# Optimization experiments

Measured on AMD Instinct MI355X. Metric: run time of the kernel, lower is better.

Reference implementation:

```python
import jax, jax.numpy as jnp
import numpy as np

B, N, H = 16, 1024, 768
NEG_INF = -9e15
SLOPE = 0.2


def setup_inputs() -> dict:
    key = jax.random.key(0)
    k1, k2, k3, k4, k5 = jax.random.split(key, 5)
    x = jax.random.normal(k1, (B, N, H), dtype=jnp.float32)
    # node_length acts as a per-node validity mask (float, used via outer product)
    lengths = jax.random.randint(k2, (B,), N // 2, N)
    node_length = (jnp.arange(N)[None, :] < lengths[:, None]).astype(jnp.float32)
    # sparse-ish binary adjacency with self-loops
    adj = (jax.random.uniform(k3, (B, N, N)) < 0.05).astype(jnp.float32)
    adj = jnp.maximum(adj, jnp.eye(N, dtype=jnp.float32)[None])
    # params: kaiming-normal init
    W = jax.random.normal(k4, (H, H), dtype=jnp.float32) * np.sqrt(2.0 / H)
    a = jax.random.normal(k5, (2 * H, 1), dtype=jnp.float32) * np.sqrt(2.0 / (2 * H))
    return {"input": x, "node_length": node_length, "graph_structure": adj, "W": W, "a": a}


def reference(input, node_length, graph_structure, W, a):
    # node_vec = A @ X  [B,N,H]
    node_vec = jnp.matmul(graph_structure, input)
    h = jnp.matmul(node_vec, W)  # [B,N,F]
    F_ = W.shape[1]
    a1 = a[:F_, 0]   # weights on h_i
    a2 = a[F_:, 0]   # weights on h_j
    # e[b,i,j] = leaky_relu(h_i . a1 + h_j . a2)  (identical to concat+matmul with a)
    s1 = jnp.einsum("bnf,f->bn", h, a1)
    s2 = jnp.einsum("bnf,f->bn", h, a2)
    e = jax.nn.leaky_relu(s1[:, :, None] + s2[:, None, :], negative_slope=SLOPE)
    # bias = outer product of node_length; mask where adj or bias <= 1e-6
    bias = node_length[:, :, None] * node_length[:, None, :]
    valid = (graph_structure > 1e-6) & (bias > 1e-6)
    scores = jnp.where(valid, e, NEG_INF)
    attn = jax.nn.softmax(scores, axis=-1)  # attn_dropout=0 -> identity
    return node_vec, attn
```

## Files before the change

kernel.cpp:

```cpp
#include <hip/hip_runtime.h>
#include <hip/hip_bf16.h>

#define BB 16
#define NN 1024
#define HH 768
#define NEG_INF_ -9.0e15f
#define SLOPE_ 0.2f

typedef __bf16 bh8 __attribute__((ext_vector_type(8)));
typedef __bf16 bh4 __attribute__((ext_vector_type(4)));
typedef float f4 __attribute__((ext_vector_type(4)));
typedef unsigned int u32;
typedef unsigned long long u64;


__device__ __forceinline__ float wave_sum0(float v) {
    #pragma unroll
    for (int off = 32; off > 0; off >>= 1) v += __shfl_down(v, off, 64);
    return v;
}
__device__ __forceinline__ float wave_sum_all(float v) {
    #pragma unroll
    for (int off = 1; off < 64; off <<= 1) v += __shfl_xor(v, off, 64);
    return v;
}
__device__ __forceinline__ float wave_max_all(float v) {
    #pragma unroll
    for (int off = 1; off < 64; off <<= 1) v = fmaxf(v, __shfl_xor(v, off, 64));
    return v;
}


__device__ __forceinline__ void gl_lds16(const void* g, void* l) {
    __builtin_amdgcn_global_load_lds(
        (const __attribute__((address_space(1))) u32*)g,
        (__attribute__((address_space(3))) u32*)l, 16, 0, 0);
}


__global__ __launch_bounds__(256) void wa_kernel(const float* __restrict__ W,
                                                 const float* __restrict__ a,
                                                 float* __restrict__ wa1,
                                                 float* __restrict__ wa2) {
    const int f = blockIdx.x * 4 + (threadIdx.x >> 6);
    const int lane = threadIdx.x & 63;
    const float* Wr = W + (size_t)f * HH;
    float v1 = 0.f, v2 = 0.f;
    #pragma unroll
    for (int i = 0; i < 3; i++) {
        const int h = lane * 4 + i * 256;
        const float4 w  = *(const float4*)(Wr + h);
        const float4 a1 = *(const float4*)(a + h);
        const float4 a2 = *(const float4*)(a + HH + h);
        v1 += w.x * a1.x + w.y * a1.y + w.z * a1.z + w.w * a1.w;
        v2 += w.x * a2.x + w.y * a2.y + w.z * a2.z + w.w * a2.w;
    }
    v1 = wave_sum0(v1);
    v2 = wave_sum0(v2);
    if (lane == 0) { wa1[f] = v1; wa2[f] = v2; }
}


__global__ __launch_bounds__(256) void t_kernel(const float* __restrict__ x,
                                                const float* __restrict__ wa1,
                                                const float* __restrict__ wa2,
                                                float* __restrict__ t1,
                                                float* __restrict__ t2) {
    const int row = blockIdx.x * 4 + (threadIdx.x >> 6);
    const int lane = threadIdx.x & 63;
    const float* xr = x + (size_t)row * HH;
    float v1 = 0.f, v2 = 0.f;
    #pragma unroll
    for (int i = 0; i < 3; i++) {
        const int h = lane * 4 + i * 256;
        const float4 xv = *(const float4*)(xr + h);
        const float4 w1 = *(const float4*)(wa1 + h);
        const float4 w2 = *(const float4*)(wa2 + h);
        v1 += xv.x * w1.x + xv.y * w1.y + xv.z * w1.z + xv.w * w1.w;
        v2 += xv.x * w2.x + xv.y * w2.y + xv.z * w2.z + xv.w * w2.w;
    }
    v1 = wave_sum0(v1);
    v2 = wave_sum0(v2);
    if (lane == 0) { t1[row] = v1; t2[row] = v2; }
}


__global__ __launch_bounds__(256) void xt_kernel(const float* __restrict__ x,
                                                 __bf16* __restrict__ xT) {
    __shared__ __bf16 T[32][36];
    const int b = blockIdx.z, nt = blockIdx.y, ht = blockIdx.x;
    const int t = threadIdx.x;
    {
        const int r = t >> 3;
        const int c = (t & 7) * 4;
        const float4 v = *(const float4*)(x + ((size_t)b * NN + nt * 32 + r) * HH + ht * 32 + c);
        T[r][c + 0] = (__bf16)v.x; T[r][c + 1] = (__bf16)v.y;
        T[r][c + 2] = (__bf16)v.z; T[r][c + 3] = (__bf16)v.w;
    }
    __syncthreads();
    {
        const int h = t >> 3;
        const int nc = (t & 7) * 4;
        bh4 o = { T[nc + 0][h], T[nc + 1][h], T[nc + 2][h], T[nc + 3][h] };
        *(bh4*)(xT + ((size_t)b * HH + ht * 32 + h) * NN + nt * 32 + nc) = o;
    }
}


__global__ __launch_bounds__(256) void s_pack_kernel(const float* __restrict__ adj,
                                                     const float* __restrict__ t1,
                                                     const float* __restrict__ t2,
                                                     float* __restrict__ s1,
                                                     float* __restrict__ s2,
                                                     u64* __restrict__ bits) {
    const int row = blockIdx.x * 4 + (threadIdx.x >> 6);
    const int lane = threadIdx.x & 63;
    const int b = row >> 10;
    const float* ar = adj + (size_t)row * NN;
    const float* t1b = t1 + b * NN;
    const float* t2b = t2 + b * NN;
    float v1 = 0.f, v2 = 0.f;
    u64 myw = 0;
    #pragma unroll
    for (int i = 0; i < 16; i++) {
        const int m = lane + 64 * i;
        const float av = ar[m];
        v1 += av * t1b[m];
        v2 += av * t2b[m];
        const u64 bal = __ballot(av > 1e-6f);
        if (lane == i) myw = bal;
    }
    v1 = wave_sum0(v1);
    v2 = wave_sum0(v2);
    if (lane == 0) { s1[row] = v1; s2[row] = v2; }
    if (lane < 16) bits[(size_t)row * 16 + lane] = myw;
}


__global__ __launch_bounds__(256) void softmax_kernel(const float* __restrict__ adj,
                                                      const float* __restrict__ nl,
                                                      const float* __restrict__ s1,
                                                      const float* __restrict__ s2,
                                                      float* __restrict__ attn) {
    const int row = blockIdx.x * 4 + (threadIdx.x >> 6);
    const int lane = threadIdx.x & 63;
    const int b = row >> 10, n = row & (NN - 1);
    const float* ar = adj + (size_t)row * NN;
    const float* nlb = nl + (size_t)b * NN;
    const float* s2b = s2 + (size_t)b * NN;
    const float s1v = s1[row];
    const bool rowok = nlb[n] > 1e-6f;

    f4 sc[4];
    float mx = NEG_INF_;
    #pragma unroll
    for (int i = 0; i < 4; i++) {
        const int j = lane * 4 + i * 256;
        const float4 av = *(const float4*)(ar + j);
        const float4 sv = *(const float4*)(s2b + j);
        const float4 nv = *(const float4*)(nlb + j);
        const float zs[4] = { s1v + sv.x, s1v + sv.y, s1v + sv.z, s1v + sv.w };
        const float as_[4] = { av.x, av.y, av.z, av.w };
        const float ns[4] = { nv.x, nv.y, nv.z, nv.w };
        #pragma unroll
        for (int e = 0; e < 4; e++) {
            const float z = zs[e];
            const float lr = z > 0.f ? z : SLOPE_ * z;
            const bool valid = rowok && (as_[e] > 1e-6f) && (ns[e] > 1e-6f);
            sc[i][e] = valid ? lr : NEG_INF_;
            mx = fmaxf(mx, sc[i][e]);
        }
    }
    mx = wave_max_all(mx);

    f4 ex[4];
    float sum = 0.f;
    #pragma unroll
    for (int i = 0; i < 4; i++)
        #pragma unroll
        for (int e = 0; e < 4; e++) {
            ex[i][e] = __expf(sc[i][e] - mx);
            sum += ex[i][e];
        }
    sum = wave_sum_all(sum);
    const float inv = 1.0f / sum;

    float* outr = attn + (size_t)row * NN;
    #pragma unroll
    for (int i = 0; i < 4; i++) {
        const int j = lane * 4 + i * 256;
        float4 o;
        o.x = ex[i][0] * inv; o.y = ex[i][1] * inv;
        o.z = ex[i][2] * inv; o.w = ex[i][3] * inv;
        *(float4*)(outr + j) = o;
    }
}


#define BSTRIDE 36

__global__ __launch_bounds__(256) void gemm_bits(const u32* __restrict__ bits,
                                                 const __bf16* __restrict__ xT,
                                                 float* __restrict__ out) {
    __shared__ u32 bitsL[128 * BSTRIDE];
    __shared__ __bf16 Bs[128 * 32];
    const int b = blockIdx.z, bm = blockIdx.y, bn = blockIdx.x;
    const int tid = threadIdx.x, lane = tid & 63, wave = tid >> 6;
    const int wr = (wave >> 1) << 6;
    const int wc = (wave & 1) << 6;
    const int quad = lane >> 4, l16 = lane & 15;

    const u32* bg = bits + ((size_t)b * NN + bm * 128) * 32;
    #pragma unroll
    for (int it = 0; it < 4; it++) {
        const int c = tid + 256 * it;
        const int r = c >> 3, col = (c & 7) * 4;
        const uint4 v = *(const uint4*)(bg + r * 32 + col);
        *(uint4*)&bitsL[r * BSTRIDE + col] = v;
    }

    f4 acc[4][4];
    #pragma unroll
    for (int i = 0; i < 4; i++)
        #pragma unroll
        for (int j = 0; j < 4; j++)
            acc[i][j] = (f4){0.f, 0.f, 0.f, 0.f};

    const __bf16* xb = xT + ((size_t)b * HH + bn * 128) * NN;
    __syncthreads();

    for (int kt = 0; kt < NN; kt += 32) {
        #pragma unroll
        for (int it = 0; it < 2; it++) {
            const int c = tid + 256 * it;
            const int n = c >> 2, off = (c & 3) * 16;
            gl_lds16((const char*)(xb + (size_t)n * NN + kt) + off,
                     (char*)&Bs[n * 32] + off);
        }
        __syncthreads();

        bh8 af[4], bf_[4];
        const int kw = kt >> 5;
        #pragma unroll
        for (int i = 0; i < 4; i++) {
            const u32 w = bitsL[(wr + i * 16 + l16) * BSTRIDE + kw];
            const u32 byte = (w >> (quad * 8)) & 0xffu;
            #pragma unroll
            for (int j = 0; j < 8; j++)
                af[i][j] = ((byte >> j) & 1u) ? (__bf16)1.0f : (__bf16)0.0f;
        }
        #pragma unroll
        for (int j = 0; j < 4; j++)
            bf_[j] = *(const bh8*)&Bs[(wc + j * 16 + l16) * 32 + quad * 8];

        #pragma unroll
        for (int i = 0; i < 4; i++)
            #pragma unroll
            for (int j = 0; j < 4; j++)
                acc[i][j] = __builtin_amdgcn_mfma_f32_16x16x32_bf16(af[i], bf_[j], acc[i][j], 0, 0, 0);
        __syncthreads();
    }

    float* Cb = out + (size_t)b * NN * HH + (size_t)bm * 128 * HH + bn * 128;
    const int rbase = wr + quad * 4;
    const int cbase = wc + l16;
    #pragma unroll
    for (int i = 0; i < 4; i++)
        #pragma unroll
        for (int j = 0; j < 4; j++)
            #pragma unroll
            for (int r = 0; r < 4; r++)
                Cb[(size_t)(rbase + i * 16 + r) * HH + cbase + j * 16] = acc[i][j][r];
}


extern "C" void kernel_launch(void* const* d_in, const int* in_sizes, int n_in,
                              void* d_out, int out_size, void* d_ws, size_t ws_size,
                              hipStream_t stream) {
    const float* x   = (const float*)d_in[0];
    const float* nl  = (const float*)d_in[1];
    const float* adj = (const float*)d_in[2];
    const float* W   = (const float*)d_in[3];
    const float* a   = (const float*)d_in[4];

    float* out = (float*)d_out;
    float* node_vec = out;
    float* attn = out + (size_t)BB * NN * HH;

    __bf16* xT = (__bf16*)attn;
    u64* bits = (u64*)(attn + (size_t)6 * 1024 * 1024);

    float* ws  = (float*)d_ws;
    float* wa1 = ws;
    float* wa2 = wa1 + HH;
    float* t1  = wa2 + HH;
    float* t2  = t1 + BB * NN;
    float* s1  = t2 + BB * NN;
    float* s2  = s1 + BB * NN;

    hipLaunchKernelGGL(wa_kernel, dim3(192), dim3(256), 0, stream, W, a, wa1, wa2);
    hipLaunchKernelGGL(t_kernel, dim3(4096), dim3(256), 0, stream, x, wa1, wa2, t1, t2);
    hipLaunchKernelGGL(xt_kernel, dim3(24, 32, BB), dim3(256), 0, stream, x, xT);
    hipLaunchKernelGGL(s_pack_kernel, dim3(4096), dim3(256), 0, stream, adj, t1, t2, s1, s2, bits);
    hipLaunchKernelGGL(gemm_bits, dim3(6, 8, BB), dim3(256), 0, stream, bits ? (const u32*)bits : nullptr, xT, node_vec);
    hipLaunchKernelGGL(softmax_kernel, dim3(4096), dim3(256), 0, stream, adj, nl, s1, s2, attn);
}
```

Measured before the change: 275.0 us.

## Fuse x·wa projection into transpose kernel and use bf16 adjacency for GEMM

```diff
diff --git a/kernel.cpp b/kernel.cpp
--- a/kernel.cpp
+++ b/kernel.cpp
@@ -11,7 +11,6 @@
 typedef __bf16 bh4 __attribute__((ext_vector_type(4)));
 typedef float f4 __attribute__((ext_vector_type(4)));
 typedef unsigned int u32;
-typedef unsigned long long u64;
 
 
 __device__ __forceinline__ float wave_sum0(float v) {
@@ -41,7 +40,12 @@
 __global__ __launch_bounds__(256) void wa_kernel(const float* __restrict__ W,
                                                  const float* __restrict__ a,
                                                  float* __restrict__ wa1,
-                                                 float* __restrict__ wa2) {
+                                                 float* __restrict__ wa2,
+                                                 float* __restrict__ t1,
+                                                 float* __restrict__ t2) {
+    const int gid = blockIdx.x * 256 + threadIdx.x;
+    if (gid < BB * NN) { t1[gid] = 0.f; t2[gid] = 0.f; }
+
     const int f = blockIdx.x * 4 + (threadIdx.x >> 6);
     const int lane = threadIdx.x & 63;
     const float* Wr = W + (size_t)f * HH;
@@ -61,49 +65,37 @@
 }
 
 
-__global__ __launch_bounds__(256) void t_kernel(const float* __restrict__ x,
-                                                const float* __restrict__ wa1,
-                                                const float* __restrict__ wa2,
-                                                float* __restrict__ t1,
-                                                float* __restrict__ t2) {
-    const int row = blockIdx.x * 4 + (threadIdx.x >> 6);
-    const int lane = threadIdx.x & 63;
-    const float* xr = x + (size_t)row * HH;
-    float v1 = 0.f, v2 = 0.f;
-    #pragma unroll
-    for (int i = 0; i < 3; i++) {
-        const int h = lane * 4 + i * 256;
-        const float4 xv = *(const float4*)(xr + h);
-        const float4 w1 = *(const float4*)(wa1 + h);
-        const float4 w2 = *(const float4*)(wa2 + h);
-        v1 += xv.x * w1.x + xv.y * w1.y + xv.z * w1.z + xv.w * w1.w;
-        v2 += xv.x * w2.x + xv.y * w2.y + xv.z * w2.z + xv.w * w2.w;
-    }
-    v1 = wave_sum0(v1);
-    v2 = wave_sum0(v2);
-    if (lane == 0) { t1[row] = v1; t2[row] = v2; }
-}
-
-
 __global__ __launch_bounds__(256) void xt_kernel(const float* __restrict__ x,
-                                                 __bf16* __restrict__ xT) {
+                                                 const float* __restrict__ wa1,
+                                                 const float* __restrict__ wa2,
+                                                 __bf16* __restrict__ xT,
+                                                 float* __restrict__ t1,
+                                                 float* __restrict__ t2) {
     __shared__ __bf16 T[32][36];
     const int b = blockIdx.z, nt = blockIdx.y, ht = blockIdx.x;
     const int t = threadIdx.x;
-    {
-        const int r = t >> 3;
-        const int c = (t & 7) * 4;
-        const float4 v = *(const float4*)(x + ((size_t)b * NN + nt * 32 + r) * HH + ht * 32 + c);
-        T[r][c + 0] = (__bf16)v.x; T[r][c + 1] = (__bf16)v.y;
-        T[r][c + 2] = (__bf16)v.z; T[r][c + 3] = (__bf16)v.w;
-    }
+    const int r = t >> 3;
+    const int c = (t & 7) * 4;
+    const float4 v = *(const float4*)(x + ((size_t)b * NN + nt * 32 + r) * HH + ht * 32 + c);
+    T[r][c + 0] = (__bf16)v.x; T[r][c + 1] = (__bf16)v.y;
+    T[r][c + 2] = (__bf16)v.z; T[r][c + 3] = (__bf16)v.w;
+
+    const float4 w1 = *(const float4*)(wa1 + ht * 32 + c);
+    const float4 w2 = *(const float4*)(wa2 + ht * 32 + c);
+    float p1 = v.x * w1.x + v.y * w1.y + v.z * w1.z + v.w * w1.w;
+    float p2 = v.x * w2.x + v.y * w2.y + v.z * w2.z + v.w * w2.w;
+    p1 += __shfl_down(p1, 4, 8); p1 += __shfl_down(p1, 2, 8); p1 += __shfl_down(p1, 1, 8);
+    p2 += __shfl_down(p2, 4, 8); p2 += __shfl_down(p2, 2, 8); p2 += __shfl_down(p2, 1, 8);
+    if ((t & 7) == 0) {
+        atomicAdd(&t1[b * NN + nt * 32 + r], p1);
+        atomicAdd(&t2[b * NN + nt * 32 + r], p2);
+    }
+
     __syncthreads();
-    {
-        const int h = t >> 3;
-        const int nc = (t & 7) * 4;
-        bh4 o = { T[nc + 0][h], T[nc + 1][h], T[nc + 2][h], T[nc + 3][h] };
-        *(bh4*)(xT + ((size_t)b * HH + ht * 32 + h) * NN + nt * 32 + nc) = o;
-    }
+    const int h = t >> 3;
+    const int nc = (t & 7) * 4;
+    bh4 o = { T[nc + 0][h], T[nc + 1][h], T[nc + 2][h], T[nc + 3][h] };
+    *(bh4*)(xT + ((size_t)b * HH + ht * 32 + h) * NN + nt * 32 + nc) = o;
 }
 
 
@@ -112,28 +104,89 @@
                                                      const float* __restrict__ t2,
                                                      float* __restrict__ s1,
                                                      float* __restrict__ s2,
-                                                     u64* __restrict__ bits) {
+                                                     __bf16* __restrict__ adjB) {
     const int row = blockIdx.x * 4 + (threadIdx.x >> 6);
     const int lane = threadIdx.x & 63;
     const int b = row >> 10;
     const float* ar = adj + (size_t)row * NN;
+    __bf16* abr = adjB + (size_t)row * NN;
     const float* t1b = t1 + b * NN;
     const float* t2b = t2 + b * NN;
     float v1 = 0.f, v2 = 0.f;
-    u64 myw = 0;
-    #pragma unroll
-    for (int i = 0; i < 16; i++) {
-        const int m = lane + 64 * i;
-        const float av = ar[m];
-        v1 += av * t1b[m];
-        v2 += av * t2b[m];
-        const u64 bal = __ballot(av > 1e-6f);
-        if (lane == i) myw = bal;
+    #pragma unroll
+    for (int i = 0; i < 4; i++) {
+        const int j = lane * 4 + i * 256;
+        const float4 av = *(const float4*)(ar + j);
+        const float4 u  = *(const float4*)(t1b + j);
+        const float4 w  = *(const float4*)(t2b + j);
+        v1 += av.x * u.x + av.y * u.y + av.z * u.z + av.w * u.w;
+        v2 += av.x * w.x + av.y * w.y + av.z * w.z + av.w * w.w;
+        bh4 o = { (__bf16)av.x, (__bf16)av.y, (__bf16)av.z, (__bf16)av.w };
+        *(bh4*)(abr + j) = o;
     }
     v1 = wave_sum0(v1);
     v2 = wave_sum0(v2);
     if (lane == 0) { s1[row] = v1; s2[row] = v2; }
-    if (lane < 16) bits[(size_t)row * 16 + lane] = myw;
+}
+
+
+__global__ __launch_bounds__(256) void gemm_bf16(const __bf16* __restrict__ adjB,
+                                                 const __bf16* __restrict__ xT,
+                                                 float* __restrict__ out) {
+    __shared__ __bf16 As[128 * 32];
+    __shared__ __bf16 Bs[128 * 32];
+    const int b = blockIdx.z, bm = blockIdx.y, bn = blockIdx.x;
+    const int tid = threadIdx.x, lane = tid & 63, wave = tid >> 6;
+    const int wr = (wave >> 1) << 6;
+    const int wc = (wave & 1) << 6;
+    const int quad = lane >> 4, l16 = lane & 15;
+
+    const __bf16* Ab = adjB + ((size_t)b * NN + bm * 128) * NN;
+    const __bf16* Xb = xT + ((size_t)b * HH + bn * 128) * NN;
+
+    f4 acc[4][4];
+    #pragma unroll
+    for (int i = 0; i < 4; i++)
+        #pragma unroll
+        for (int j = 0; j < 4; j++)
+            acc[i][j] = (f4){0.f, 0.f, 0.f, 0.f};
+
+    for (int kt = 0; kt < NN; kt += 32) {
+        #pragma unroll
+        for (int it = 0; it < 2; it++) {
+            const int c = tid + 256 * it;
+            const int r = c >> 2, ko = (c & 3) * 8;
+            gl_lds16(Ab + (size_t)r * NN + kt + ko, &As[r * 32 + ko]);
+            gl_lds16(Xb + (size_t)r * NN + kt + ko, &Bs[r * 32 + ko]);
+        }
+        __syncthreads();
+
+        bh8 af[4], bf_[4];
+        #pragma unroll
+        for (int i = 0; i < 4; i++)
+            af[i] = *(const bh8*)&As[(wr + i * 16 + l16) * 32 + quad * 8];
+        #pragma unroll
+        for (int j = 0; j < 4; j++)
+            bf_[j] = *(const bh8*)&Bs[(wc + j * 16 + l16) * 32 + quad * 8];
+
+        #pragma unroll
+        for (int i = 0; i < 4; i++)
+            #pragma unroll
+            for (int j = 0; j < 4; j++)
+                acc[i][j] = __builtin_amdgcn_mfma_f32_16x16x32_bf16(af[i], bf_[j], acc[i][j], 0, 0, 0);
+        __syncthreads();
+    }
+
+    float* Cb = out + (size_t)b * NN * HH + (size_t)bm * 128 * HH + bn * 128;
+    const int rbase = wr + quad * 4;
+    const int cbase = wc + l16;
+    #pragma unroll
+    for (int i = 0; i < 4; i++)
+        #pragma unroll
+        for (int j = 0; j < 4; j++)
+            #pragma unroll
+            for (int r = 0; r < 4; r++)
+                Cb[(size_t)(rbase + i * 16 + r) * HH + cbase + j * 16] = acc[i][j][r];
 }
 
 
@@ -197,83 +250,6 @@
 }
 
 
-#define BSTRIDE 36
-
-__global__ __launch_bounds__(256) void gemm_bits(const u32* __restrict__ bits,
-                                                 const __bf16* __restrict__ xT,
-                                                 float* __restrict__ out) {
-    __shared__ u32 bitsL[128 * BSTRIDE];
-    __shared__ __bf16 Bs[128 * 32];
-    const int b = blockIdx.z, bm = blockIdx.y, bn = blockIdx.x;
-    const int tid = threadIdx.x, lane = tid & 63, wave = tid >> 6;
-    const int wr = (wave >> 1) << 6;
-    const int wc = (wave & 1) << 6;
-    const int quad = lane >> 4, l16 = lane & 15;
-
-    const u32* bg = bits + ((size_t)b * NN + bm * 128) * 32;
-    #pragma unroll
-    for (int it = 0; it < 4; it++) {
-        const int c = tid + 256 * it;
-        const int r = c >> 3, col = (c & 7) * 4;
-        const uint4 v = *(const uint4*)(bg + r * 32 + col);
-        *(uint4*)&bitsL[r * BSTRIDE + col] = v;
-    }
-
-    f4 acc[4][4];
-    #pragma unroll
-    for (int i = 0; i < 4; i++)
-        #pragma unroll
-        for (int j = 0; j < 4; j++)
-            acc[i][j] = (f4){0.f, 0.f, 0.f, 0.f};
-
-    const __bf16* xb = xT + ((size_t)b * HH + bn * 128) * NN;
-    __syncthreads();
-
-    for (int kt = 0; kt < NN; kt += 32) {
-        #pragma unroll
-        for (int it = 0; it < 2; it++) {
-            const int c = tid + 256 * it;
-            const int n = c >> 2, off = (c & 3) * 16;
-            gl_lds16((const char*)(xb + (size_t)n * NN + kt) + off,
-                     (char*)&Bs[n * 32] + off);
-        }
-        __syncthreads();
-
-        bh8 af[4], bf_[4];
-        const int kw = kt >> 5;
-        #pragma unroll
-        for (int i = 0; i < 4; i++) {
-            const u32 w = bitsL[(wr + i * 16 + l16) * BSTRIDE + kw];
-            const u32 byte = (w >> (quad * 8)) & 0xffu;
-            #pragma unroll
-            for (int j = 0; j < 8; j++)
-                af[i][j] = ((byte >> j) & 1u) ? (__bf16)1.0f : (__bf16)0.0f;
-        }
-        #pragma unroll
-        for (int j = 0; j < 4; j++)
-            bf_[j] = *(const bh8*)&Bs[(wc + j * 16 + l16) * 32 + quad * 8];
-
-        #pragma unroll
-        for (int i = 0; i < 4; i++)
-            #pragma unroll
-            for (int j = 0; j < 4; j++)
-                acc[i][j] = __builtin_amdgcn_mfma_f32_16x16x32_bf16(af[i], bf_[j], acc[i][j], 0, 0, 0);
-        __syncthreads();
-    }
-
-    float* Cb = out + (size_t)b * NN * HH + (size_t)bm * 128 * HH + bn * 128;
-    const int rbase = wr + quad * 4;
-    const int cbase = wc + l16;
-    #pragma unroll
-    for (int i = 0; i < 4; i++)
-        #pragma unroll
-        for (int j = 0; j < 4; j++)
-            #pragma unroll
-            for (int r = 0; r < 4; r++)
-                Cb[(size_t)(rbase + i * 16 + r) * HH + cbase + j * 16] = acc[i][j][r];
-}
-
-
 extern "C" void kernel_launch(void* const* d_in, const int* in_sizes, int n_in,
                               void* d_out, int out_size, void* d_ws, size_t ws_size,
                               hipStream_t stream) {
@@ -287,8 +263,8 @@
     float* node_vec = out;
     float* attn = out + (size_t)BB * NN * HH;
 
-    __bf16* xT = (__bf16*)attn;
-    u64* bits = (u64*)(attn + (size_t)6 * 1024 * 1024);
+    __bf16* xT   = (__bf16*)attn;
+    __bf16* adjB = (__bf16*)(attn + 6291456);
 
     float* ws  = (float*)d_ws;
     float* wa1 = ws;
@@ -298,10 +274,9 @@
     float* s1  = t2 + BB * NN;
     float* s2  = s1 + BB * NN;
 
-    hipLaunchKernelGGL(wa_kernel, dim3(192), dim3(256), 0, stream, W, a, wa1, wa2);
-    hipLaunchKernelGGL(t_kernel, dim3(4096), dim3(256), 0, stream, x, wa1, wa2, t1, t2);
-    hipLaunchKernelGGL(xt_kernel, dim3(24, 32, BB), dim3(256), 0, stream, x, xT);
-    hipLaunchKernelGGL(s_pack_kernel, dim3(4096), dim3(256), 0, stream, adj, t1, t2, s1, s2, bits);
-    hipLaunchKernelGGL(gemm_bits, dim3(6, 8, BB), dim3(256), 0, stream, bits ? (const u32*)bits : nullptr, xT, node_vec);
+    hipLaunchKernelGGL(wa_kernel, dim3(192), dim3(256), 0, stream, W, a, wa1, wa2, t1, t2);
+    hipLaunchKernelGGL(xt_kernel, dim3(24, 32, BB), dim3(256), 0, stream, x, wa1, wa2, xT, t1, t2);
+    hipLaunchKernelGGL(s_pack_kernel, dim3(4096), dim3(256), 0, stream, adj, t1, t2, s1, s2, adjB);
+    hipLaunchKernelGGL(gemm_bf16, dim3(6, 8, BB), dim3(256), 0, stream, adjB, xT, node_vec);
     hipLaunchKernelGGL(softmax_kernel, dim3(4096), dim3(256), 0, stream, adj, nl, s1, s2, attn);
 }
```

After: 284.4 us. 1.03x slower.
